# Kernel optimization log

Measured on AMD Instinct MI355X. Metric: run time of the kernel, lower is better.

The kernel has to match this reference:

```python
import jax, jax.numpy as jnp
import numpy as np

MPPI_ITER = 6
HORIZON = 18
NUM_SAMPLES = 65536
ACTION_DIM = 4
NUM_ELITES = 64
STD = 0.5
MOMENTUM = 0.1
TEMPERATURE = 1.0


def setup_inputs() -> dict:
    key = jax.random.key(0)
    k1, k2, k3 = jax.random.split(key, 3)
    pi_actions = jax.random.normal(k1, (HORIZON, NUM_SAMPLES, ACTION_DIM), dtype=jnp.float32)
    noise = jax.random.normal(k2, (MPPI_ITER, HORIZON, NUM_SAMPLES, ACTION_DIM), dtype=jnp.float32)
    target = jax.random.normal(k3, (HORIZON, ACTION_DIM), dtype=jnp.float32)
    return {"pi_actions": pi_actions, "noise": noise, "target": target}


def _value(actions, target):
    # Surrogate for methods.estimate_value: quadratic trajectory cost.
    # actions: [H, N, A], target: [H, A] -> value: [N]
    return -jnp.sum((actions - target[:, None, :]) ** 2, axis=(0, 2))


def reference(pi_actions, noise, target):
    H, N, A = pi_actions.shape
    mean = pi_actions[:, 0, :]                      # [H, A]
    std = jnp.ones((H, A), dtype=pi_actions.dtype)  # [H, A]
    elite_actions = pi_actions[:, :NUM_ELITES, :]
    for i in range(MPPI_ITER):
        # sample CEM trajectories around (mean, std), clamp to action bounds
        cem_actions = jnp.clip(
            mean[:, None, :] + STD * std[:, None, :] * noise[i], -4.0, 4.0
        )                                                      # [H, N, A]
        actions = jnp.concatenate([pi_actions, cem_actions], axis=1)  # [H, 2N, A]
        value = _value(actions, target)                        # [2N]
        elite_value, elite_idxs = jax.lax.top_k(value, NUM_ELITES)    # [E]
        elite_actions = actions[:, elite_idxs, :]              # [H, E, A]
        # exp-weighted reweighting (faithful double normalization of `score`)
        max_value = jnp.max(elite_value)
        score = jnp.exp(TEMPERATURE * (elite_value - max_value))
        score = score / jnp.sum(score)
        ssum = jnp.sum(score)
        _mean = jnp.sum(score[None, :, None] * elite_actions, axis=1) / (ssum + 1e-9)
        _std = jnp.sqrt(
            jnp.sum(score[None, :, None] * (elite_actions - _mean[:, None, :]) ** 2, axis=1)
            / (ssum + 1e-9)
        )
        # faithful reproduction of clamp_(horizon, 2): min=18 > max=2 -> pins to 2
        _std = jnp.clip(_std, float(H), 2.0)
        mean = MOMENTUM * mean + (1.0 - MOMENTUM) * _mean
        std = _std
    a = elite_actions[:, 0, :]  # best elite action sequence [H, A]
    return a
```

## Files before the change

### kernel.cpp

```cpp
#include <hip/hip_runtime.h>
#include <math.h>

#define H 18
#define NS 65536
#define AD 4
#define HAD 72
#define ITERS 6
#define DELTA 16.0f
#define SCAP 4096
#define NCH 2048

__device__ __forceinline__ unsigned encf(float f) {
    unsigned u = __float_as_uint(f);
    return (u & 0x80000000u) ? ~u : (u | 0x80000000u);
}
__device__ __forceinline__ float decf(unsigned u) {
    return __uint_as_float((u & 0x80000000u) ? (u & 0x7FFFFFFFu) : ~u);
}
__device__ __forceinline__ float clamp4f(float x) { return fminf(fmaxf(x, -4.0f), 4.0f); }
__device__ __forceinline__ unsigned long long packkey(float v, unsigned idx) {
    return ((unsigned long long)encf(v) << 32) | (unsigned long long)(~idx);
}

#define QH0(q) ((q) == 0 ? 0 : (q) == 1 ? 5 : (q) == 2 ? 10 : 14)
#define QCN(q) ((q) < 2 ? 5 : 4)

__global__ void __launch_bounds__(256, 4) k_value0(
        const float4* __restrict__ pi4, const float4* __restrict__ nz4,
        const float* __restrict__ target, float* __restrict__ meanarr,
        float* __restrict__ v_pi, float* __restrict__ wmax_pi,
        float* __restrict__ v_c0, float* __restrict__ wmax_c0) {
    __shared__ float tgt[HAD], mnL[HAD];
    __shared__ float smaxc[4], smaxp[4];
    const int tid = threadIdx.x, wg = blockIdx.x;
    const int lane = tid & 63, wid = tid >> 6;
    const int q = lane >> 4, s = lane & 15;
    const int n = wg * 64 + wid * 16 + s;
    const int h0 = QH0(q), cnt = QCN(q);

    float4 xs0 = nz4[(size_t)(h0 + 0) * NS + n];
    float4 xs1 = nz4[(size_t)(h0 + 1) * NS + n];
    float4 xs2 = nz4[(size_t)(h0 + 2) * NS + n];
    float4 xs3 = nz4[(size_t)(h0 + 3) * NS + n];
    const int h4 = (h0 + 4 > 17) ? 17 : h0 + 4;
    float4 xs4 = nz4[(size_t)h4 * NS + n];
    float4 ps0 = pi4[(size_t)(h0 + 0) * NS + n];
    float4 ps1 = pi4[(size_t)(h0 + 1) * NS + n];
    float4 ps2 = pi4[(size_t)(h0 + 2) * NS + n];
    float4 ps3 = pi4[(size_t)(h0 + 3) * NS + n];
    float4 ps4 = pi4[(size_t)h4 * NS + n];

    if (tid < HAD) {
        tgt[tid] = target[tid];
        float m0 = ((const float*)pi4)[(size_t)(tid >> 2) * NS * AD + (tid & 3)];
        mnL[tid] = m0;
        meanarr[tid] = m0;
    }
    __syncthreads();

    const float w4 = (cnt == 5) ? 1.0f : 0.0f;
    float a2 = 0.f, p2 = 0.f;
    {
        float c; int h;
        h = h0 + 0;
        c = clamp4f(mnL[h*4+0] + 0.5f*xs0.x) - tgt[h*4+0]; a2 += c*c;
        c = clamp4f(mnL[h*4+1] + 0.5f*xs0.y) - tgt[h*4+1]; a2 += c*c;
        c = clamp4f(mnL[h*4+2] + 0.5f*xs0.z) - tgt[h*4+2]; a2 += c*c;
        c = clamp4f(mnL[h*4+3] + 0.5f*xs0.w) - tgt[h*4+3]; a2 += c*c;
        c = ps0.x - tgt[h*4+0]; p2 += c*c;  c = ps0.y - tgt[h*4+1]; p2 += c*c;
        c = ps0.z - tgt[h*4+2]; p2 += c*c;  c = ps0.w - tgt[h*4+3]; p2 += c*c;
        h = h0 + 1;
        c = clamp4f(mnL[h*4+0] + 0.5f*xs1.x) - tgt[h*4+0]; a2 += c*c;
        c = clamp4f(mnL[h*4+1] + 0.5f*xs1.y) - tgt[h*4+1]; a2 += c*c;
        c = clamp4f(mnL[h*4+2] + 0.5f*xs1.z) - tgt[h*4+2]; a2 += c*c;
        c = clamp4f(mnL[h*4+3] + 0.5f*xs1.w) - tgt[h*4+3]; a2 += c*c;
        c = ps1.x - tgt[h*4+0]; p2 += c*c;  c = ps1.y - tgt[h*4+1]; p2 += c*c;
        c = ps1.z - tgt[h*4+2]; p2 += c*c;  c = ps1.w - tgt[h*4+3]; p2 += c*c;
        h = h0 + 2;
        c = clamp4f(mnL[h*4+0] + 0.5f*xs2.x) - tgt[h*4+0]; a2 += c*c;
        c = clamp4f(mnL[h*4+1] + 0.5f*xs2.y) - tgt[h*4+1]; a2 += c*c;
        c = clamp4f(mnL[h*4+2] + 0.5f*xs2.z) - tgt[h*4+2]; a2 += c*c;
        c = clamp4f(mnL[h*4+3] + 0.5f*xs2.w) - tgt[h*4+3]; a2 += c*c;
        c = ps2.x - tgt[h*4+0]; p2 += c*c;  c = ps2.y - tgt[h*4+1]; p2 += c*c;
        c = ps2.z - tgt[h*4+2]; p2 += c*c;  c = ps2.w - tgt[h*4+3]; p2 += c*c;
        h = h0 + 3;
        c = clamp4f(mnL[h*4+0] + 0.5f*xs3.x) - tgt[h*4+0]; a2 += c*c;
        c = clamp4f(mnL[h*4+1] + 0.5f*xs3.y) - tgt[h*4+1]; a2 += c*c;
        c = clamp4f(mnL[h*4+2] + 0.5f*xs3.z) - tgt[h*4+2]; a2 += c*c;
        c = clamp4f(mnL[h*4+3] + 0.5f*xs3.w) - tgt[h*4+3]; a2 += c*c;
        c = ps3.x - tgt[h*4+0]; p2 += c*c;  c = ps3.y - tgt[h*4+1]; p2 += c*c;
        c = ps3.z - tgt[h*4+2]; p2 += c*c;  c = ps3.w - tgt[h*4+3]; p2 += c*c;
        h = h4;
        c = clamp4f(mnL[h*4+0] + 0.5f*xs4.x) - tgt[h*4+0]; a2 += w4*c*c;
        c = clamp4f(mnL[h*4+1] + 0.5f*xs4.y) - tgt[h*4+1]; a2 += w4*c*c;
        c = clamp4f(mnL[h*4+2] + 0.5f*xs4.z) - tgt[h*4+2]; a2 += w4*c*c;
        c = clamp4f(mnL[h*4+3] + 0.5f*xs4.w) - tgt[h*4+3]; a2 += w4*c*c;
        c = ps4.x - tgt[h*4+0]; p2 += w4*c*c;  c = ps4.y - tgt[h*4+1]; p2 += w4*c*c;
        c = ps4.z - tgt[h*4+2]; p2 += w4*c*c;  c = ps4.w - tgt[h*4+3]; p2 += w4*c*c;
    }
    a2 += __shfl_xor(a2, 16);  a2 += __shfl_xor(a2, 32);
    p2 += __shfl_xor(p2, 16);  p2 += __shfl_xor(p2, 32);
    const float vc = -a2, vp = -p2;
    if (lane < 16) { v_c0[n] = vc; v_pi[n] = vp; }
    float mc = vc, mp = vp;
#pragma unroll
    for (int off = 8; off; off >>= 1) {
        mc = fmaxf(mc, __shfl_xor(mc, off));
        mp = fmaxf(mp, __shfl_xor(mp, off));
    }
    if (lane == 0) { smaxc[wid] = mc; smaxp[wid] = mp; }
    __syncthreads();
    if (tid == 0) {
        wmax_c0[wg * 2 + 0] = fmaxf(smaxc[0], smaxc[1]);
        wmax_c0[wg * 2 + 1] = fmaxf(smaxc[2], smaxc[3]);
        wmax_pi[wg * 2 + 0] = fmaxf(smaxp[0], smaxp[1]);
        wmax_pi[wg * 2 + 1] = fmaxf(smaxp[2], smaxp[3]);
    }
}

__global__ void __launch_bounds__(256, 4) k_value(
        const float4* __restrict__ nz4, const float* __restrict__ target,
        const float* __restrict__ meanarr_i,
        float* __restrict__ v_out, float* __restrict__ wmax_out) {
    __shared__ float tgt[HAD], mnL[HAD];
    __shared__ float smax[4];
    const int tid = threadIdx.x, wg = blockIdx.x;
    const int lane = tid & 63, wid = tid >> 6;
    const int q = lane >> 4, s = lane & 15;
    const int n = wg * 64 + wid * 16 + s;
    const int h0 = QH0(q), cnt = QCN(q);

    float4 xs0 = nz4[(size_t)(h0 + 0) * NS + n];
    float4 xs1 = nz4[(size_t)(h0 + 1) * NS + n];
    float4 xs2 = nz4[(size_t)(h0 + 2) * NS + n];
    float4 xs3 = nz4[(size_t)(h0 + 3) * NS + n];
    const int h4 = (h0 + 4 > 17) ? 17 : h0 + 4;
    float4 xs4 = nz4[(size_t)h4 * NS + n];

    if (tid < HAD) { tgt[tid] = target[tid]; mnL[tid] = meanarr_i[tid]; }
    __syncthreads();

    const float w4 = (cnt == 5) ? 1.0f : 0.0f;
    float a2 = 0.f;
    {
        float c; int h;
        h = h0 + 0;
        c = clamp4f(mnL[h*4+0] + xs0.x) - tgt[h*4+0]; a2 += c*c;
        c = clamp4f(mnL[h*4+1] + xs0.y) - tgt[h*4+1]; a2 += c*c;
        c = clamp4f(mnL[h*4+2] + xs0.z) - tgt[h*4+2]; a2 += c*c;
        c = clamp4f(mnL[h*4+3] + xs0.w) - tgt[h*4+3]; a2 += c*c;
        h = h0 + 1;
        c = clamp4f(mnL[h*4+0] + xs1.x) - tgt[h*4+0]; a2 += c*c;
        c = clamp4f(mnL[h*4+1] + xs1.y) - tgt[h*4+1]; a2 += c*c;
        c = clamp4f(mnL[h*4+2] + xs1.z) - tgt[h*4+2]; a2 += c*c;
        c = clamp4f(mnL[h*4+3] + xs1.w) - tgt[h*4+3]; a2 += c*c;
        h = h0 + 2;
        c = clamp4f(mnL[h*4+0] + xs2.x) - tgt[h*4+0]; a2 += c*c;
        c = clamp4f(mnL[h*4+1] + xs2.y) - tgt[h*4+1]; a2 += c*c;
        c = clamp4f(mnL[h*4+2] + xs2.z) - tgt[h*4+2]; a2 += c*c;
        c = clamp4f(mnL[h*4+3] + xs2.w) - tgt[h*4+3]; a2 += c*c;
        h = h0 + 3;
        c = clamp4f(mnL[h*4+0] + xs3.x) - tgt[h*4+0]; a2 += c*c;
        c = clamp4f(mnL[h*4+1] + xs3.y) - tgt[h*4+1]; a2 += c*c;
        c = clamp4f(mnL[h*4+2] + xs3.z) - tgt[h*4+2]; a2 += c*c;
        c = clamp4f(mnL[h*4+3] + xs3.w) - tgt[h*4+3]; a2 += c*c;
        h = h4;
        c = clamp4f(mnL[h*4+0] + xs4.x) - tgt[h*4+0]; a2 += w4*c*c;
        c = clamp4f(mnL[h*4+1] + xs4.y) - tgt[h*4+1]; a2 += w4*c*c;
        c = clamp4f(mnL[h*4+2] + xs4.z) - tgt[h*4+2]; a2 += w4*c*c;
        c = clamp4f(mnL[h*4+3] + xs4.w) - tgt[h*4+3]; a2 += w4*c*c;
    }
    a2 += __shfl_xor(a2, 16);  a2 += __shfl_xor(a2, 32);
    const float vc = -a2;
    if (lane < 16) v_out[n] = vc;
    float m = vc;
#pragma unroll
    for (int off = 8; off; off >>= 1) m = fmaxf(m, __shfl_xor(m, off));
    if (lane == 0) smax[wid] = m;
    __syncthreads();
    if (tid == 0) {
        wmax_out[wg * 2 + 0] = fmaxf(smax[0], smax[1]);
        wmax_out[wg * 2 + 1] = fmaxf(smax[2], smax[3]);
    }
}

__global__ void __launch_bounds__(1024) k_reduce(
        const float* __restrict__ pi, const float* __restrict__ noise_i,
        float* __restrict__ meanarr,
        const float* __restrict__ wmax_pi, const float* __restrict__ v_pi,
        const float* __restrict__ wmax_c, const float* __restrict__ v_c,
        float* __restrict__ out, int iter, int is_last) {
    __shared__ unsigned long long skey[SCAP];
    __shared__ unsigned long long top[64];
    __shared__ unsigned long long redk[16];
    __shared__ float buf[64 * 76];
    __shared__ float w64[64];
    __shared__ float mprev[HAD];
    __shared__ float redf[16];
    __shared__ unsigned s_fcnt;
    __shared__ float s_S, s_gmax;
    const int tid = threadIdx.x, lane = tid & 63, wid = tid >> 6;

    if (tid < HAD) mprev[tid] = meanarr[iter * HAD + tid];
    if (tid == 0) s_fcnt = 0u;
    __syncthreads();

    {
        float g = fmaxf(fmaxf(wmax_pi[tid], wmax_pi[tid + 1024]),
                        fmaxf(wmax_c[tid], wmax_c[tid + 1024]));
        for (int off = 32; off; off >>= 1) g = fmaxf(g, __shfl_xor(g, off));
        if (lane == 0) redf[wid] = g;
        __syncthreads();
        if (tid == 0) {
            float x = redf[0];
            for (int q = 1; q < 16; ++q) x = fmaxf(x, redf[q]);
            s_gmax = x;
        }
        __syncthreads();
    }
    const float gmax = s_gmax, thr = gmax - DELTA;

#pragma unroll
    for (int r = 0; r < 2; ++r) {
        const int c = tid + r * 1024;
        if (wmax_pi[c] >= thr) {
            const float4* v4 = (const float4*)v_pi + c * 8;
            for (int q = 0; q < 8; ++q) {
                float4 x = v4[q];
                float vv[4] = {x.x, x.y, x.z, x.w};
#pragma unroll
                for (int c2 = 0; c2 < 4; ++c2)
                    if (vv[c2] >= thr) {
                        unsigned p = atomicAdd(&s_fcnt, 1u);
                        if (p < SCAP) skey[p] = packkey(vv[c2], (unsigned)(c * 32 + q * 4 + c2));
                    }
            }
        }
        if (wmax_c[c] >= thr) {
            const float4* v4 = (const float4*)v_c + c * 8;
            for (int q = 0; q < 8; ++q) {
                float4 x = v4[q];
                float vv[4] = {x.x, x.y, x.z, x.w};
#pragma unroll
                for (int c2 = 0; c2 < 4; ++c2)
                    if (vv[c2] >= thr) {
                        unsigned p = atomicAdd(&s_fcnt, 1u);
                        if (p < SCAP) skey[p] = packkey(vv[c2], (unsigned)(NS + c * 32 + q * 4 + c2));
                    }
            }
        }
    }
    __syncthreads();
    unsigned fc = s_fcnt; if (fc > SCAP) fc = SCAP;
    const float pscale = (iter == 0) ? 0.5f : 1.0f;

    if (is_last) {
        unsigned long long bk = 0ull;
        for (unsigned k = tid; k < fc; k += 1024) if (skey[k] > bk) bk = skey[k];
        for (int off = 32; off; off >>= 1) {
            unsigned long long ok = __shfl_xor(bk, off);
            if (ok > bk) bk = ok;
        }
        if (lane == 0) redk[wid] = bk;
        __syncthreads();
        if (tid == 0) {
            unsigned long long b = redk[0];
            for (int q = 1; q < 16; ++q) if (redk[q] > b) b = redk[q];
            redk[0] = b;
        }
        __syncthreads();
        const unsigned idx = (unsigned)~(unsigned)(redk[0] & 0xFFFFFFFFull);
        if (tid < HAD) {
            const int h = tid >> 2, aa = tid & 3;
            float o;
            if (idx < NS) o = pi[(size_t)h * NS * AD + (size_t)idx * AD + aa];
            else o = clamp4f(mprev[tid] + pscale * noise_i[(size_t)h * NS * AD + (size_t)(idx - NS) * AD + aa]);
            out[tid] = o;
        }
        return;
    }

    int E;
    if (fc <= 64u) {
        if (tid < 64) top[tid] = (tid < (int)fc) ? skey[tid] : 0ull;
        __syncthreads();
        E = (int)fc;
    } else {
        unsigned P2 = 128; while (P2 < fc) P2 <<= 1;
        for (unsigned k = fc + tid; k < P2; k += 1024) skey[k] = 0ull;
        __syncthreads();
        for (unsigned kk = 2; kk <= P2; kk <<= 1) {
            for (unsigned j = kk >> 1; j; j >>= 1) {
                for (unsigned x = tid; x < P2; x += 1024) {
                    unsigned l = x ^ j;
                    if (l > x) {
                        unsigned long long k0 = skey[x], k1 = skey[l];
                        bool desc = ((x & kk) == 0);
                        if (desc ? (k0 < k1) : (k0 > k1)) { skey[x] = k1; skey[l] = k0; }
                    }
                }
                __syncthreads();
            }
        }
        if (tid < 64) top[tid] = skey[tid];
        __syncthreads();
        E = 64;
    }

    if (tid < 64) {
        float we = (tid < E) ? expf(decf((unsigned)(top[tid] >> 32)) - gmax) : 0.0f;
        w64[tid] = we;
        float s = we;
        for (int off = 32; off; off >>= 1) s += __shfl_xor(s, off);
        if (tid == 0) s_S = s;
    }
    __syncthreads();
    const float invS = 1.0f / (s_S * (1.0f + 1e-9f));

    const float4* pi4 = (const float4*)pi;
    const float4* nz4 = (const float4*)noise_i;
    for (int el = tid; el < 64 * H; el += 1024) {
        const int e = el / H, h = el - e * H;
        float ax = 0.f, ay = 0.f, az = 0.f, aw = 0.f;
        if (e < E) {
            const unsigned idx = (unsigned)~(unsigned)(top[e] & 0xFFFFFFFFull);
            float4 a;
            if (idx < NS) {
                a = pi4[(size_t)h * NS + idx];
            } else {
                float4 nz = nz4[(size_t)h * NS + (idx - NS)];
                a.x = clamp4f(mprev[h*4+0] + pscale * nz.x);
                a.y = clamp4f(mprev[h*4+1] + pscale * nz.y);
                a.z = clamp4f(mprev[h*4+2] + pscale * nz.z);
                a.w = clamp4f(mprev[h*4+3] + pscale * nz.w);
            }
            const float we = w64[e];
            ax = we * a.x; ay = we * a.y; az = we * a.z; aw = we * a.w;
        }
        buf[e * 76 + h * 4 + 0] = ax;
        buf[e * 76 + h * 4 + 1] = ay;
        buf[e * 76 + h * 4 + 2] = az;
        buf[e * 76 + h * 4 + 3] = aw;
    }
    __syncthreads();
    if (tid < HAD) {
        float s = 0.f;
#pragma unroll 8
        for (int e = 0; e < 64; ++e) s += buf[e * 76 + tid];
        meanarr[(iter + 1) * HAD + tid] = 0.1f * mprev[tid] + 0.9f * (s * invS);
    }
}

extern "C" void kernel_launch(void* const* d_in, const int* in_sizes, int n_in,
                              void* d_out, int out_size, void* d_ws, size_t ws_size,
                              hipStream_t stream) {
    const float* pi     = (const float*)d_in[0];
    const float* noise  = (const float*)d_in[1];
    const float* target = (const float*)d_in[2];
    float* out = (float*)d_out;

    float* ws = (float*)d_ws;
    float* meanarr = ws;
    float* wmax_pi = ws + 1024;
    float* wmax_c  = wmax_pi + NCH;
    float* v_pi    = wmax_c + 6 * NCH;
    float* v_c     = v_pi + NS;

    k_value0<<<1024, 256, 0, stream>>>((const float4*)pi, (const float4*)noise,
                                       target, meanarr, v_pi, wmax_pi, v_c, wmax_c);
    for (int i = 0; i < ITERS - 1; ++i) {
        const float* nzi = noise + (size_t)i * H * NS * AD;
        k_reduce<<<1, 1024, 0, stream>>>(pi, nzi, meanarr, wmax_pi, v_pi,
                                         wmax_c + (size_t)i * NCH,
                                         v_c + (size_t)i * NS, out, i, 0);
        const float* nzn = noise + (size_t)(i + 1) * H * NS * AD;
        k_value<<<1024, 256, 0, stream>>>((const float4*)nzn, target,
                                          meanarr + (size_t)(i + 1) * HAD,
                                          v_c + (size_t)(i + 1) * NS,
                                          wmax_c + (size_t)(i + 1) * NCH);
    }
    k_reduce<<<1, 1024, 0, stream>>>(pi, noise + (size_t)5 * H * NS * AD, meanarr,
                                     wmax_pi, v_pi,
                                     wmax_c + (size_t)5 * NCH,
                                     v_c + (size_t)5 * NS, out, 5, 1);
}
```

Before: 157.7 us.

## Pick elite threshold via per-chunk max histogram and use rank-based top-64 selection

Builds a shared-memory histogram of chunk maxima below the global max and picks a tighter threshold so that at least 64 chunks qualify. This shrinks the candidate set scanned and collected. The bitonic sort of candidates is replaced by an O(fc^2) rank count in which each candidate computes its rank and writes itself into the top-64 slot if it ranks below 64. The approach depends on candidate counts staying small and on the keys being distinct, which the packed index guarantees.

```diff
diff --git a/kernel.cpp b/kernel.cpp
--- a/kernel.cpp
+++ b/kernel.cpp
@@ -9,6 +9,8 @@
 #define DELTA 16.0f
 #define SCAP 4096
 #define NCH 2048
+#define NBIN 128
+#define BINW 0.125f
 
 __device__ __forceinline__ unsigned encf(float f) {
     unsigned u = __float_as_uint(f);
@@ -197,17 +199,20 @@
     __shared__ float w64[64];
     __shared__ float mprev[HAD];
     __shared__ float redf[16];
+    __shared__ unsigned hist[NBIN];
     __shared__ unsigned s_fcnt;
-    __shared__ float s_S, s_gmax;
+    __shared__ float s_S, s_gmax, s_thr;
     const int tid = threadIdx.x, lane = tid & 63, wid = tid >> 6;
 
     if (tid < HAD) mprev[tid] = meanarr[iter * HAD + tid];
     if (tid == 0) s_fcnt = 0u;
-    __syncthreads();
-
-    {
-        float g = fmaxf(fmaxf(wmax_pi[tid], wmax_pi[tid + 1024]),
-                        fmaxf(wmax_c[tid], wmax_c[tid + 1024]));
+    if (tid < NBIN) hist[tid] = 0u;
+    __syncthreads();
+
+    const float m0 = wmax_pi[tid], m1 = wmax_pi[tid + 1024];
+    const float m2 = wmax_c[tid],  m3 = wmax_c[tid + 1024];
+    {
+        float g = fmaxf(fmaxf(m0, m1), fmaxf(m2, m3));
         for (int off = 32; off; off >>= 1) g = fmaxf(g, __shfl_xor(g, off));
         if (lane == 0) redf[wid] = g;
         __syncthreads();
@@ -218,35 +223,49 @@
         }
         __syncthreads();
     }
-    const float gmax = s_gmax, thr = gmax - DELTA;
-
-#pragma unroll
-    for (int r = 0; r < 2; ++r) {
-        const int c = tid + r * 1024;
-        if (wmax_pi[c] >= thr) {
-            const float4* v4 = (const float4*)v_pi + c * 8;
-            for (int q = 0; q < 8; ++q) {
-                float4 x = v4[q];
-                float vv[4] = {x.x, x.y, x.z, x.w};
-#pragma unroll
-                for (int c2 = 0; c2 < 4; ++c2)
-                    if (vv[c2] >= thr) {
-                        unsigned p = atomicAdd(&s_fcnt, 1u);
-                        if (p < SCAP) skey[p] = packkey(vv[c2], (unsigned)(c * 32 + q * 4 + c2));
-                    }
+    const float gmax = s_gmax;
+
+    {
+        float mm[4] = {m0, m1, m2, m3};
+#pragma unroll
+        for (int r = 0; r < 4; ++r) {
+            if (mm[r] >= gmax - DELTA) {
+                int b = (int)((gmax - mm[r]) * (1.0f / BINW));
+                if (b > NBIN - 1) b = NBIN - 1;
+                atomicAdd(&hist[b], 1u);
             }
         }
-        if (wmax_c[c] >= thr) {
-            const float4* v4 = (const float4*)v_c + c * 8;
-            for (int q = 0; q < 8; ++q) {
-                float4 x = v4[q];
-                float vv[4] = {x.x, x.y, x.z, x.w};
-#pragma unroll
-                for (int c2 = 0; c2 < 4; ++c2)
-                    if (vv[c2] >= thr) {
-                        unsigned p = atomicAdd(&s_fcnt, 1u);
-                        if (p < SCAP) skey[p] = packkey(vv[c2], (unsigned)(NS + c * 32 + q * 4 + c2));
-                    }
+    }
+    __syncthreads();
+    if (tid == 0) {
+        unsigned cum = 0; int bstar = NBIN - 1;
+        for (int b = 0; b < NBIN; ++b) {
+            cum += hist[b];
+            if (cum >= 64u) { bstar = b; break; }
+        }
+        s_thr = gmax - (float)(bstar + 1) * BINW;
+    }
+    __syncthreads();
+    const float thr = s_thr;
+
+    {
+        const float mm[4] = {m0, m1, m2, m3};
+#pragma unroll
+        for (int r = 0; r < 4; ++r) {
+            if (mm[r] >= thr) {
+                const int c = (r & 1) ? (tid + 1024) : tid;
+                const float4* v4 = ((r < 2) ? (const float4*)v_pi : (const float4*)v_c) + c * 8;
+                const unsigned base = ((r < 2) ? 0u : (unsigned)NS) + (unsigned)(c * 32);
+                for (int qq = 0; qq < 8; ++qq) {
+                    float4 x = v4[qq];
+                    float vv[4] = {x.x, x.y, x.z, x.w};
+#pragma unroll
+                    for (int c2 = 0; c2 < 4; ++c2)
+                        if (vv[c2] >= thr) {
+                            unsigned p = atomicAdd(&s_fcnt, 1u);
+                            if (p < SCAP) skey[p] = packkey(vv[c2], base + qq * 4 + c2);
+                        }
+                }
             }
         }
     }
@@ -286,23 +305,12 @@
         __syncthreads();
         E = (int)fc;
     } else {
-        unsigned P2 = 128; while (P2 < fc) P2 <<= 1;
-        for (unsigned k = fc + tid; k < P2; k += 1024) skey[k] = 0ull;
-        __syncthreads();
-        for (unsigned kk = 2; kk <= P2; kk <<= 1) {
-            for (unsigned j = kk >> 1; j; j >>= 1) {
-                for (unsigned x = tid; x < P2; x += 1024) {
-                    unsigned l = x ^ j;
-                    if (l > x) {
-                        unsigned long long k0 = skey[x], k1 = skey[l];
-                        bool desc = ((x & kk) == 0);
-                        if (desc ? (k0 < k1) : (k0 > k1)) { skey[x] = k1; skey[l] = k0; }
-                    }
-                }
-                __syncthreads();
-            }
-        }
-        if (tid < 64) top[tid] = skey[tid];
+        for (unsigned i = tid; i < fc; i += 1024) {
+            unsigned long long k = skey[i];
+            unsigned r = 0;
+            for (unsigned j = 0; j < fc; ++j) r += (skey[j] > k) ? 1u : 0u;
+            if (r < 64u) top[r] = k;
+        }
         __syncthreads();
         E = 64;
     }
```

Measured after the change: 129.8 us, median of 2. 1.21x faster.
